# Optimization experiments

Measured on AMD Instinct MI355X. Metric: run time of the kernel, lower is better.

Reference implementation:

```python
import jax, jax.numpy as jnp
import numpy as np

N_STACK = 1
SEL_RATE = 0.5


def setup_inputs() -> dict:
    key = jax.random.key(0)
    k1, k2, k3 = jax.random.split(key, 3)
    preds = jax.random.normal(k1, (128, 17, 64, 64), dtype=jnp.float32)
    targets = jax.random.normal(k2, (2, 128, 17, 64, 64), dtype=jnp.float32)
    sampleWeight = jax.random.uniform(k3, (128, 1), dtype=jnp.float32)
    return {"preds": preds, "targets": targets, "sampleWeight": sampleWeight}


def _score_and_thr(v):
    # v: [bs, k, HW]; softmax over joints (dim=-2), max over spatial, global
    # (1 - selRate)-quantile threshold via sort, as in the torch code.
    sm = jax.nn.softmax(v, axis=-2)
    score = jnp.max(sm, axis=-1)                      # [bs, k]
    flat = jnp.sort(score.reshape(-1))
    thr = flat[int(flat.shape[0] * (1.0 - SEL_RATE))]  # scalar
    mask = (score >= thr).astype(v.dtype)             # [bs, k]
    return score, thr, mask


def reference(preds, targets, sampleWeight):
    bs, k = preds.shape[0], preds.shape[1]
    # ensemble mean over models -> pseudo target [bs, k, H, W]
    targets_mean = jnp.mean(targets, axis=0)
    v1 = preds.reshape(bs, k, -1)
    v2 = targets_mean.reshape(bs, k, -1)

    # per-(sample, joint) MSE, weighted
    loss = jnp.mean((v1 - v2) ** 2, axis=-1)          # [bs, k]
    loss = loss * sampleWeight                        # sampleWeight [bs,1] broadcast

    v1_score, thr1, v1_mask = _score_and_thr(v1)
    v2_score, thr2, v2_mask = _score_and_thr(v2)
    mask = v1_mask * v2_mask                          # [bs, k]

    num_pseudo = jnp.sum(loss.reshape(-1) > 0).astype(jnp.int32)
    num_selected = jnp.sum(mask.reshape(-1) > 0).astype(jnp.int32)

    # masked mean over unlabeled samples (sampleWeight > 0) instead of
    # Python-loop filtering: identical math when >=1 positive sample.
    w = (sampleWeight[:, 0] > 0).astype(v1_score.dtype)  # [bs]
    cnt = jnp.sum(w)
    v1_mean = jnp.sum(v1_score * w[:, None], axis=0) / cnt  # [k]
    v2_mean = jnp.sum(v2_score * w[:, None], axis=0) / cnt  # [k]
    joint_score_mean = 0.5 * (v1_mean + v2_mean)             # [k]

    combined_loss = jnp.sum(loss * mask)
    rateThr1 = thr1[None]
    rateThr2 = thr2[None]
    return combined_loss, num_pseudo, num_selected, joint_score_mean, rateThr1, rateThr2
```

## Files before the change

kernel.cpp:

```cpp
#include <hip/hip_runtime.h>

#define BS 128
#define KJ 17
#define HW 4096
#define CHUNKS 16
#define NBLK1 (BS * CHUNKS)
#define NBK (BS * KJ)
#define KSEL 1088

#define PL_OFF 0
#define S1_OFF (NBLK1 * KJ)
#define S2_OFF (2 * NBLK1 * KJ)
#define LW_OFF (3 * NBLK1 * KJ)
#define SA_OFF (LW_OFF + NBK)
#define SB_OFF (SA_OFF + NBK)
#define THR_OFF (SB_OFF + NBK)

template<int K0, int NK>
__device__ __forceinline__ void team_work(const float* __restrict__ pb,
                                          const float* __restrict__ t0b,
                                          const float* __restrict__ t1b,
                                          int ti, float (*lb)[132],
                                          float2* ep, float2* et,
                                          float2& spP, float2& spT) {
    float2 pv[NK], va[NK], vb[NK];
#pragma unroll
    for (int j = 0; j < NK; ++j) pv[j] = *(const float2*)(pb + (K0 + j) * HW);
#pragma unroll
    for (int j = 0; j < NK; ++j) va[j] = *(const float2*)(t0b + (K0 + j) * HW);
#pragma unroll
    for (int j = 0; j < NK; ++j) vb[j] = *(const float2*)(t1b + (K0 + j) * HW);
    spP = make_float2(0.f, 0.f);
    spT = make_float2(0.f, 0.f);
#pragma unroll
    for (int j = 0; j < NK; ++j) {
        float2 tv;
        tv.x = 0.5f * (va[j].x + vb[j].x);
        tv.y = 0.5f * (va[j].y + vb[j].y);
        const float dx = pv[j].x - tv.x, dy = pv[j].y - tv.y;
        lb[K0 + j][ti] = dx * dx + dy * dy;
        float2 e1, e2;
        e1.x = __expf(pv[j].x); e1.y = __expf(pv[j].y);
        e2.x = __expf(tv.x);    e2.y = __expf(tv.y);
        ep[j] = e1; et[j] = e2;
        spP.x += e1.x; spP.y += e1.y;
        spT.x += e2.x; spT.y += e2.y;
    }
}

__global__ __launch_bounds__(256, 4) void k1_reduce(const float* __restrict__ preds,
                                                    const float* __restrict__ targets,
                                                    float* __restrict__ ws) {
    __shared__ float lb[KJ][132];
    __shared__ float2 sP[2][128];
    __shared__ float2 sT[2][128];
    __shared__ float buf2[KJ][4];

    const int bid = blockIdx.x;
    const int b = bid >> 4;
    const int c = bid & 15;
    const int tid = threadIdx.x;
    const int tm = tid >> 7;
    const int ti = tid & 127;
    const int s0 = (c << 8) | (ti << 1);

    const float* pb  = preds   + (size_t)b * KJ * HW + s0;
    const float* t0b = targets + (size_t)b * KJ * HW + s0;
    const float* t1b = targets + (size_t)(BS + b) * KJ * HW + s0;

    float2 ep[9], et[9], spP, spT;
    if (tm == 0) team_work<0, 9>(pb, t0b, t1b, ti, lb, ep, et, spP, spT);
    else         team_work<9, 8>(pb, t0b, t1b, ti, lb, ep, et, spP, spT);
    sP[tm][ti] = spP;
    sT[tm][ti] = spT;
    __syncthreads();

    float2 invP, invT;
    invP.x = 1.0f / (sP[0][ti].x + sP[1][ti].x);
    invP.y = 1.0f / (sP[0][ti].y + sP[1][ti].y);
    invT.x = 1.0f / (sT[0][ti].x + sT[1][ti].x);
    invT.y = 1.0f / (sT[0][ti].y + sT[1][ti].y);

    if (tid < KJ * 4) {
        const int k = tid >> 2, seg = tid & 3;
        float r = 0.f;
#pragma unroll
        for (int i = 0; i < 32; ++i) {
            const int idx = (i + seg * 8) & 31;
            r += lb[k][(seg << 5) + idx];
        }
        buf2[k][seg] = r;
    }
    __syncthreads();

    if (tid < KJ) {
        float r = buf2[tid][0] + buf2[tid][1] + buf2[tid][2] + buf2[tid][3];
        ws[PL_OFF + bid * KJ + tid] = r;
    }
    if (tm == 0) {
#pragma unroll
        for (int j = 0; j < 9; ++j)
            lb[j][ti] = fmaxf(ep[j].x * invP.x, ep[j].y * invP.y);
    } else {
#pragma unroll
        for (int j = 0; j < 8; ++j)
            lb[9 + j][ti] = fmaxf(ep[j].x * invP.x, ep[j].y * invP.y);
    }
    __syncthreads();

    if (tid < KJ * 4) {
        const int k = tid >> 2, seg = tid & 3;
        float r = 0.f;
#pragma unroll
        for (int i = 0; i < 32; ++i) {
            const int idx = (i + seg * 8) & 31;
            r = fmaxf(r, lb[k][(seg << 5) + idx]);
        }
        buf2[k][seg] = r;
    }
    __syncthreads();

    if (tid < KJ) {
        float r = fmaxf(fmaxf(buf2[tid][0], buf2[tid][1]),
                        fmaxf(buf2[tid][2], buf2[tid][3]));
        ws[S1_OFF + bid * KJ + tid] = r;
    }
    if (tm == 0) {
#pragma unroll
        for (int j = 0; j < 9; ++j)
            lb[j][ti] = fmaxf(et[j].x * invT.x, et[j].y * invT.y);
    } else {
#pragma unroll
        for (int j = 0; j < 8; ++j)
            lb[9 + j][ti] = fmaxf(et[j].x * invT.x, et[j].y * invT.y);
    }
    __syncthreads();

    if (tid < KJ * 4) {
        const int k = tid >> 2, seg = tid & 3;
        float r = 0.f;
#pragma unroll
        for (int i = 0; i < 32; ++i) {
            const int idx = (i + seg * 8) & 31;
            r = fmaxf(r, lb[k][(seg << 5) + idx]);
        }
        buf2[k][seg] = r;
    }
    __syncthreads();

    if (tid < KJ) {
        float r = fmaxf(fmaxf(buf2[tid][0], buf2[tid][1]),
                        fmaxf(buf2[tid][2], buf2[tid][3]));
        ws[S2_OFF + bid * KJ + tid] = r;
    }
}

__global__ __launch_bounds__(256) void k2_fold(float* __restrict__ ws,
                                               const float* __restrict__ sw) {
    const int e = blockIdx.x * 256 + threadIdx.x;
    if (e >= NBK) return;
    const int b = e / KJ;
    const int k = e - b * KJ;
    float L = 0.f, S1 = 0.f, S2 = 0.f;
#pragma unroll
    for (int c = 0; c < CHUNKS; ++c) {
        const int idx = (b * CHUNKS + c) * KJ + k;
        L += ws[PL_OFF + idx];
        S1 = fmaxf(S1, ws[S1_OFF + idx]);
        S2 = fmaxf(S2, ws[S2_OFF + idx]);
    }
    ws[LW_OFF + e] = L * (1.0f / HW) * sw[b];
    ws[SA_OFF + e] = S1;
    ws[SB_OFF + e] = S2;
}

__global__ __launch_bounds__(256) void k3_select(float* __restrict__ ws) {
    const int w = blockIdx.x * 4 + (threadIdx.x >> 6);
    const int lane = threadIdx.x & 63;
    const int arr = (w >= NBK) ? 1 : 0;
    const int cand = w - arr * NBK;
    const float* sc = ws + (arr ? SB_OFF : SA_OFF);
    const float e = sc[cand];
    int clt = 0, cle = 0;
    for (int j = lane; j < NBK; j += 64) {
        float x = sc[j];
        clt += (x < e) ? 1 : 0;
        cle += (x <= e) ? 1 : 0;
    }
#pragma unroll
    for (int off = 32; off > 0; off >>= 1) {
        clt += __shfl_xor(clt, off, 64);
        cle += __shfl_xor(cle, off, 64);
    }
    if (lane == 0 && clt <= KSEL && KSEL < cle) {
        ws[THR_OFF + arr] = e;
    }
}

__global__ __launch_bounds__(256) void k4_final(const float* __restrict__ ws,
                                                const float* __restrict__ sw,
                                                float* __restrict__ out) {
    const int tid = threadIdx.x;
    const float thrA = ws[THR_OFF + 0];
    const float thrB = ws[THR_OFF + 1];

    float comb = 0.f, np = 0.f, ns = 0.f;
    for (int e = tid; e < NBK; e += 256) {
        const float L  = ws[LW_OFF + e];
        const float s1 = ws[SA_OFF + e];
        const float s2 = ws[SB_OFF + e];
        const float m = (s1 >= thrA && s2 >= thrB) ? 1.f : 0.f;
        comb += L * m;
        np += (L > 0.f) ? 1.f : 0.f;
        ns += m;
    }
#pragma unroll
    for (int off = 32; off > 0; off >>= 1) {
        comb += __shfl_xor(comb, off, 64);
        np   += __shfl_xor(np, off, 64);
        ns   += __shfl_xor(ns, off, 64);
    }
    __shared__ float wr[4][3];
    const int wid = tid >> 6, lane = tid & 63;
    if (lane == 0) { wr[wid][0] = comb; wr[wid][1] = np; wr[wid][2] = ns; }
    __syncthreads();
    if (tid == 0) {
        float C = 0.f, NP = 0.f, NS = 0.f;
#pragma unroll
        for (int i = 0; i < 4; ++i) { C += wr[i][0]; NP += wr[i][1]; NS += wr[i][2]; }
        out[0] = C;
        out[1] = NP;
        out[2] = NS;
        out[20] = thrA;
        out[21] = thrB;
    }
    if (tid < KJ) {
        float a1 = 0.f, a2 = 0.f, cnt = 0.f;
        for (int b = 0; b < BS; ++b) {
            const float wf = (sw[b] > 0.f) ? 1.f : 0.f;
            cnt += wf;
            a1 += ws[SA_OFF + b * KJ + tid] * wf;
            a2 += ws[SB_OFF + b * KJ + tid] * wf;
        }
        out[3 + tid] = 0.5f * (a1 + a2) / cnt;
    }
}

extern "C" void kernel_launch(void* const* d_in, const int* in_sizes, int n_in,
                              void* d_out, int out_size, void* d_ws, size_t ws_size,
                              hipStream_t stream) {
    const float* preds   = (const float*)d_in[0];
    const float* targets = (const float*)d_in[1];
    const float* sw      = (const float*)d_in[2];
    float* out = (float*)d_out;
    float* ws  = (float*)d_ws;

    hipLaunchKernelGGL(k1_reduce, dim3(NBLK1), dim3(256), 0, stream, preds, targets, ws);
    hipLaunchKernelGGL(k2_fold, dim3((NBK + 255) / 256), dim3(256), 0, stream, ws, sw);
    hipLaunchKernelGGL(k3_select, dim3((2 * NBK) / 4), dim3(256), 0, stream, ws);
    hipLaunchKernelGGL(k4_final, dim3(1), dim3(256), 0, stream, ws, sw, out);
}
```

Before: 39.31 us.

## Use float4 loads with four joint-teams and recompute exps instead of storing

The first kernel now has each thread load float4 (four spatial points) instead of float2, and the block is split into four teams of 64 threads that each handle about four joints, instead of two teams handling eight or nine. Rather than keeping the exponentials in registers for the score pass, it keeps the raw inputs and recomputes __expf when writing the scores. The shared-memory partial-reduction buffers shrink to match. This is meant to widen memory transactions and cut register pressure, at the cost of computing extra exponentials.

After: 40.24 us. 1.02x slower.

```diff
diff --git a/kernel.cpp b/kernel.cpp
--- a/kernel.cpp
+++ b/kernel.cpp
@@ -17,141 +17,150 @@
 #define THR_OFF (SB_OFF + NBK)
 
 template<int K0, int NK>
-__device__ __forceinline__ void team_work(const float* __restrict__ pb,
-                                          const float* __restrict__ t0b,
-                                          const float* __restrict__ t1b,
-                                          int ti, float (*lb)[132],
-                                          float2* ep, float2* et,
-                                          float2& spP, float2& spT) {
-    float2 pv[NK], va[NK], vb[NK];
-#pragma unroll
-    for (int j = 0; j < NK; ++j) pv[j] = *(const float2*)(pb + (K0 + j) * HW);
-#pragma unroll
-    for (int j = 0; j < NK; ++j) va[j] = *(const float2*)(t0b + (K0 + j) * HW);
-#pragma unroll
-    for (int j = 0; j < NK; ++j) vb[j] = *(const float2*)(t1b + (K0 + j) * HW);
-    spP = make_float2(0.f, 0.f);
-    spT = make_float2(0.f, 0.f);
+__device__ __forceinline__ void team_pass1(const float* __restrict__ pb,
+                                           const float* __restrict__ t0b,
+                                           const float* __restrict__ t1b,
+                                           int ti, float (*lb)[68],
+                                           float4* pv, float4* tv,
+                                           float4& spP, float4& spT) {
+    float4 vb[NK];
+#pragma unroll
+    for (int j = 0; j < NK; ++j) pv[j] = *(const float4*)(pb + (K0 + j) * HW);
+#pragma unroll
+    for (int j = 0; j < NK; ++j) tv[j] = *(const float4*)(t0b + (K0 + j) * HW);
+#pragma unroll
+    for (int j = 0; j < NK; ++j) vb[j] = *(const float4*)(t1b + (K0 + j) * HW);
+    spP = make_float4(0.f, 0.f, 0.f, 0.f);
+    spT = make_float4(0.f, 0.f, 0.f, 0.f);
 #pragma unroll
     for (int j = 0; j < NK; ++j) {
-        float2 tv;
-        tv.x = 0.5f * (va[j].x + vb[j].x);
-        tv.y = 0.5f * (va[j].y + vb[j].y);
-        const float dx = pv[j].x - tv.x, dy = pv[j].y - tv.y;
-        lb[K0 + j][ti] = dx * dx + dy * dy;
-        float2 e1, e2;
-        e1.x = __expf(pv[j].x); e1.y = __expf(pv[j].y);
-        e2.x = __expf(tv.x);    e2.y = __expf(tv.y);
-        ep[j] = e1; et[j] = e2;
-        spP.x += e1.x; spP.y += e1.y;
-        spT.x += e2.x; spT.y += e2.y;
+        tv[j].x = 0.5f * (tv[j].x + vb[j].x);
+        tv[j].y = 0.5f * (tv[j].y + vb[j].y);
+        tv[j].z = 0.5f * (tv[j].z + vb[j].z);
+        tv[j].w = 0.5f * (tv[j].w + vb[j].w);
+        const float dx = pv[j].x - tv[j].x, dy = pv[j].y - tv[j].y;
+        const float dz = pv[j].z - tv[j].z, dw = pv[j].w - tv[j].w;
+        lb[K0 + j][ti] = dx * dx + dy * dy + dz * dz + dw * dw;
+        spP.x += __expf(pv[j].x); spP.y += __expf(pv[j].y);
+        spP.z += __expf(pv[j].z); spP.w += __expf(pv[j].w);
+        spT.x += __expf(tv[j].x); spT.y += __expf(tv[j].y);
+        spT.z += __expf(tv[j].z); spT.w += __expf(tv[j].w);
+    }
+}
+
+template<int K0, int NK>
+__device__ __forceinline__ void score_write(float (*lb)[68], int ti,
+                                            const float4* v, float4 inv) {
+#pragma unroll
+    for (int j = 0; j < NK; ++j) {
+        const float m = fmaxf(fmaxf(__expf(v[j].x) * inv.x, __expf(v[j].y) * inv.y),
+                              fmaxf(__expf(v[j].z) * inv.z, __expf(v[j].w) * inv.w));
+        lb[K0 + j][ti] = m;
     }
 }
 
 __global__ __launch_bounds__(256, 4) void k1_reduce(const float* __restrict__ preds,
                                                     const float* __restrict__ targets,
                                                     float* __restrict__ ws) {
-    __shared__ float lb[KJ][132];
-    __shared__ float2 sP[2][128];
-    __shared__ float2 sT[2][128];
+    __shared__ float lb[KJ][68];
+    __shared__ float4 sP[4][64];
+    __shared__ float4 sT[4][64];
     __shared__ float buf2[KJ][4];
 
     const int bid = blockIdx.x;
     const int b = bid >> 4;
     const int c = bid & 15;
     const int tid = threadIdx.x;
-    const int tm = tid >> 7;
-    const int ti = tid & 127;
-    const int s0 = (c << 8) | (ti << 1);
+    const int tm = tid >> 6;
+    const int ti = tid & 63;
+    const int s0 = (c << 8) | (ti << 2);
 
     const float* pb  = preds   + (size_t)b * KJ * HW + s0;
     const float* t0b = targets + (size_t)b * KJ * HW + s0;
     const float* t1b = targets + (size_t)(BS + b) * KJ * HW + s0;
 
-    float2 ep[9], et[9], spP, spT;
-    if (tm == 0) team_work<0, 9>(pb, t0b, t1b, ti, lb, ep, et, spP, spT);
-    else         team_work<9, 8>(pb, t0b, t1b, ti, lb, ep, et, spP, spT);
+    float4 pv[5], tv[5], spP, spT;
+    if      (tm == 0) team_pass1<0, 4>(pb, t0b, t1b, ti, lb, pv, tv, spP, spT);
+    else if (tm == 1) team_pass1<4, 4>(pb, t0b, t1b, ti, lb, pv, tv, spP, spT);
+    else if (tm == 2) team_pass1<8, 4>(pb, t0b, t1b, ti, lb, pv, tv, spP, spT);
+    else              team_pass1<12, 5>(pb, t0b, t1b, ti, lb, pv, tv, spP, spT);
     sP[tm][ti] = spP;
     sT[tm][ti] = spT;
     __syncthreads();
 
-    float2 invP, invT;
-    invP.x = 1.0f / (sP[0][ti].x + sP[1][ti].x);
-    invP.y = 1.0f / (sP[0][ti].y + sP[1][ti].y);
-    invT.x = 1.0f / (sT[0][ti].x + sT[1][ti].x);
-    invT.y = 1.0f / (sT[0][ti].y + sT[1][ti].y);
+    float4 invP, invT;
+    {
+        const float4 a0 = sP[0][ti], a1 = sP[1][ti], a2 = sP[2][ti], a3 = sP[3][ti];
+        invP.x = 1.0f / (a0.x + a1.x + a2.x + a3.x);
+        invP.y = 1.0f / (a0.y + a1.y + a2.y + a3.y);
+        invP.z = 1.0f / (a0.z + a1.z + a2.z + a3.z);
+        invP.w = 1.0f / (a0.w + a1.w + a2.w + a3.w);
+        const float4 b0 = sT[0][ti], b1 = sT[1][ti], b2 = sT[2][ti], b3 = sT[3][ti];
+        invT.x = 1.0f / (b0.x + b1.x + b2.x + b3.x);
+        invT.y = 1.0f / (b0.y + b1.y + b2.y + b3.y);
+        invT.z = 1.0f / (b0.z + b1.z + b2.z + b3.z);
+        invT.w = 1.0f / (b0.w + b1.w + b2.w + b3.w);
+    }
 
     if (tid < KJ * 4) {
         const int k = tid >> 2, seg = tid & 3;
         float r = 0.f;
 #pragma unroll
-        for (int i = 0; i < 32; ++i) {
-            const int idx = (i + seg * 8) & 31;
-            r += lb[k][(seg << 5) + idx];
+        for (int i = 0; i < 16; ++i) {
+            const int idx = (i + seg * 4) & 15;
+            r += lb[k][(seg << 4) + idx];
         }
         buf2[k][seg] = r;
     }
     __syncthreads();
 
     if (tid < KJ) {
-        float r = buf2[tid][0] + buf2[tid][1] + buf2[tid][2] + buf2[tid][3];
-        ws[PL_OFF + bid * KJ + tid] = r;
-    }
-    if (tm == 0) {
-#pragma unroll
-        for (int j = 0; j < 9; ++j)
-            lb[j][ti] = fmaxf(ep[j].x * invP.x, ep[j].y * invP.y);
-    } else {
-#pragma unroll
-        for (int j = 0; j < 8; ++j)
-            lb[9 + j][ti] = fmaxf(ep[j].x * invP.x, ep[j].y * invP.y);
-    }
+        ws[PL_OFF + bid * KJ + tid] =
+            buf2[tid][0] + buf2[tid][1] + buf2[tid][2] + buf2[tid][3];
+    }
+    if      (tm == 0) score_write<0, 4>(lb, ti, pv, invP);
+    else if (tm == 1) score_write<4, 4>(lb, ti, pv, invP);
+    else if (tm == 2) score_write<8, 4>(lb, ti, pv, invP);
+    else              score_write<12, 5>(lb, ti, pv, invP);
     __syncthreads();
 
     if (tid < KJ * 4) {
         const int k = tid >> 2, seg = tid & 3;
         float r = 0.f;
 #pragma unroll
-        for (int i = 0; i < 32; ++i) {
-            const int idx = (i + seg * 8) & 31;
-            r = fmaxf(r, lb[k][(seg << 5) + idx]);
+        for (int i = 0; i < 16; ++i) {
+            const int idx = (i + seg * 4) & 15;
+            r = fmaxf(r, lb[k][(seg << 4) + idx]);
         }
         buf2[k][seg] = r;
     }
     __syncthreads();
 
     if (tid < KJ) {
-        float r = fmaxf(fmaxf(buf2[tid][0], buf2[tid][1]),
-                        fmaxf(buf2[tid][2], buf2[tid][3]));
-        ws[S1_OFF + bid * KJ + tid] = r;
-    }
-    if (tm == 0) {
-#pragma unroll
-        for (int j = 0; j < 9; ++j)
-            lb[j][ti] = fmaxf(et[j].x * invT.x, et[j].y * invT.y);
-    } else {
-#pragma unroll
-        for (int j = 0; j < 8; ++j)
-            lb[9 + j][ti] = fmaxf(et[j].x * invT.x, et[j].y * invT.y);
-    }
+        ws[S1_OFF + bid * KJ + tid] = fmaxf(fmaxf(buf2[tid][0], buf2[tid][1]),
+                                            fmaxf(buf2[tid][2], buf2[tid][3]));
+    }
+    if      (tm == 0) score_write<0, 4>(lb, ti, tv, invT);
+    else if (tm == 1) score_write<4, 4>(lb, ti, tv, invT);
+    else if (tm == 2) score_write<8, 4>(lb, ti, tv, invT);
+    else              score_write<12, 5>(lb, ti, tv, invT);
     __syncthreads();
 
     if (tid < KJ * 4) {
         const int k = tid >> 2, seg = tid & 3;
         float r = 0.f;
 #pragma unroll
-        for (int i = 0; i < 32; ++i) {
-            const int idx = (i + seg * 8) & 31;
-            r = fmaxf(r, lb[k][(seg << 5) + idx]);
+        for (int i = 0; i < 16; ++i) {
+            const int idx = (i + seg * 4) & 15;
+            r = fmaxf(r, lb[k][(seg << 4) + idx]);
         }
         buf2[k][seg] = r;
     }
     __syncthreads();
 
     if (tid < KJ) {
-        float r = fmaxf(fmaxf(buf2[tid][0], buf2[tid][1]),
-                        fmaxf(buf2[tid][2], buf2[tid][3]));
-        ws[S2_OFF + bid * KJ + tid] = r;
+        ws[S2_OFF + bid * KJ + tid] = fmaxf(fmaxf(buf2[tid][0], buf2[tid][1]),
+                                            fmaxf(buf2[tid][2], buf2[tid][3]));
     }
 }
 
```
